# Optimization experiments

Measured on AMD Instinct MI355X. Metric: run time of the kernel, lower is better.

The kernel has to match this reference:

```python
import jax, jax.numpy as jnp
import numpy as np

CLASS_NUM = 31
KERNEL_MUL = 2.0
KERNEL_NUM = 5


def setup_inputs() -> dict:
    key = jax.random.key(0)
    k1, k2, k3, k4 = jax.random.split(key, 4)
    B, D = 4096, 512
    source = jax.random.normal(k1, (B, D), dtype=jnp.float32)
    target = jax.random.normal(k2, (B, D), dtype=jnp.float32)
    s_label = jax.random.randint(k3, (B,), 0, CLASS_NUM)
    t_label = jax.random.uniform(k4, (B, CLASS_NUM), dtype=jnp.float32)
    return {"source": source, "target": target, "s_label": s_label, "t_label": t_label}


def _cal_weight(s_label, t_label):
    # Faithful port of the numpy weight computation (detached in the original).
    C = CLASS_NUM
    s_onehot = jax.nn.one_hot(s_label, C, dtype=jnp.float32)          # [Bs, C]
    s_sum = s_onehot.sum(axis=0)
    s_vec = s_onehot / jnp.where(s_sum == 0, 1e9, s_sum)
    t_pred = jnp.argmax(t_label, axis=1)
    t_sum = t_label.sum(axis=0)
    t_vec = t_label / jnp.where(t_sum == 0, 1.0, t_sum)
    # classes present in BOTH source labels and target argmax predictions
    s_present = s_onehot.sum(axis=0) > 0
    t_present = jax.nn.one_hot(t_pred, C, dtype=jnp.float32).sum(axis=0) > 0
    mask = (s_present & t_present).astype(jnp.float32)                # [C]
    s_vec = s_vec * mask
    t_vec = t_vec * mask
    length = mask.sum()
    inv_len = jnp.where(length > 0, 1.0 / length, 0.0)
    w_ss = (s_vec @ s_vec.T) * inv_len
    w_tt = (t_vec @ t_vec.T) * inv_len
    w_st = (s_vec @ t_vec.T) * inv_len
    w_ts = (t_vec @ s_vec.T) * inv_len
    return w_ss, w_tt, w_st, w_ts


def _gaussian_kernel(source, target):
    n = source.shape[0] + target.shape[0]
    total = jnp.concatenate([source, target], axis=0)                 # [n, d]
    # Gram-matrix trick for pairwise squared L2 (avoids n x n x d intermediate)
    sq = jnp.sum(total * total, axis=1)                               # [n]
    L2 = jnp.maximum(sq[:, None] + sq[None, :] - 2.0 * (total @ total.T), 0.0)
    bandwidth = jax.lax.stop_gradient(jnp.sum(L2)) / (n * n - n)      # .data -> detach
    bandwidth = bandwidth / (KERNEL_MUL ** (KERNEL_NUM // 2))
    kernels = jnp.zeros_like(L2)
    for i in range(KERNEL_NUM):
        kernels = kernels + jnp.exp(-L2 / (bandwidth * KERNEL_MUL ** i))
    return kernels


def reference(source, target, s_label, t_label):
    B = source.shape[0]
    w_ss, w_tt, w_st, w_ts = _cal_weight(s_label, t_label)
    w_ss = jax.lax.stop_gradient(w_ss)
    w_tt = jax.lax.stop_gradient(w_tt)
    w_st = jax.lax.stop_gradient(w_st)
    w_ts = jax.lax.stop_gradient(w_ts)
    kernels = _gaussian_kernel(source, target)
    SS = kernels[:B, :B]
    TT = kernels[B:, B:]
    ST = kernels[:B, B:]
    TS = kernels[B:, :B]
    loss = (jnp.sum(w_ss * SS) + jnp.sum(w_tt * TT)
            - jnp.sum(w_st * ST) - jnp.sum(w_ts * TS))
    # original returns 0 if the kernel matrix contains NaNs
    return jnp.where(jnp.any(jnp.isnan(kernels)), 0.0, loss)
```

## Files before the change

kernel.cpp:

```cpp
#include <hip/hip_runtime.h>

#define N_TOT 8192
#define BHALF 4096
#define D 512
#define C 31
#define QS 21.166666666666668f
#define C2 0.0044644089288178575f

typedef float f32x16 __attribute__((ext_vector_type(16)));
typedef int   i32x16 __attribute__((ext_vector_type(16)));
typedef int   i32x4  __attribute__((ext_vector_type(4)));
typedef __bf16 bf16x8 __attribute__((ext_vector_type(8)));

__device__ __forceinline__ uint bf16_rne(uint u) {
  return (u + 0x7fffu + ((u >> 16) & 1u)) >> 16;
}
__device__ __forceinline__ void split2(float x, uint& h, uint& lo) {
  uint u = __float_as_uint(x);
  h = bf16_rne(u);
  float hf = __uint_as_float(h << 16);
  lo = bf16_rne(__float_as_uint(x - hf));
}
__device__ __forceinline__ void gll16(const void* g, void* s) {
  __builtin_amdgcn_global_load_lds(
      (const __attribute__((address_space(1))) unsigned int*)g,
      (__attribute__((address_space(3))) unsigned int*)s, 16, 0, 0);
}
__device__ __forceinline__ uint pack4(const float* x, int o) {
  uint r = 0;
  #pragma unroll
  for (int b = 0; b < 4; ++b) {
    float xs = x[o + b] * QS;
    xs = fmaxf(fminf(xs, 127.f), -127.f);
    int q = __float2int_rn(xs);
    r |= (uint)(q & 255) << (8 * b);
  }
  return r;
}

__global__ __launch_bounds__(256) void k_split(const float* __restrict__ src,
                                               const float* __restrict__ tgt,
                                               const float* __restrict__ tl,
                                               uchar* __restrict__ qG,
                                               float* __restrict__ sqp,
                                               float* __restrict__ tsum_p,
                                               int* __restrict__ pres_p) {
  __shared__ float lsq[4][32];
  __shared__ float ts[C];
  __shared__ int pr[32];
  int tid = threadIdx.x, l = tid & 63, wid = tid >> 6;
  int bx = (int)blockIdx.x;
  if (bx < 1024) {
    int rg = bx >> 2;
    int kb = bx & 3;
    int ksg = kb * 4 + wid;
    int row = rg * 32 + (l & 31);
    int k0 = ksg * 32 + (l >> 5) * 16;
    const float* p = (row < BHALF) ? src + (size_t)row * D : tgt + (size_t)(row - BHALF) * D;
    float x[16];
    #pragma unroll
    for (int q = 0; q < 4; ++q) {
      float4 v = *(const float4*)(p + k0 + q * 4);
      x[q*4+0] = v.x; x[q*4+1] = v.y; x[q*4+2] = v.z; x[q*4+3] = v.w;
    }
    uint4 o = make_uint4(pack4(x, 0), pack4(x, 4), pack4(x, 8), pack4(x, 12));
    *(uint4*)(qG + (((size_t)rg * 16 + ksg) * 64 + l) * 16) = o;
    float s = 0.f;
    #pragma unroll
    for (int j = 0; j < 16; ++j) s = fmaf(x[j], x[j], s);
    s += __shfl_xor(s, 32);
    if (l < 32) lsq[wid][l] = s;
    __syncthreads();
    if (tid < 32) {
      float t = lsq[0][tid] + lsq[1][tid] + lsq[2][tid] + lsq[3][tid];
      sqp[kb * 8192 + rg * 32 + tid] = t;
    }
  } else {
    int b = bx - 1024;
    if (tid < 32) { pr[tid] = 0; if (tid < C) ts[tid] = 0.f; }
    __syncthreads();
    int base = b * 128 * C;
    for (int idx = tid; idx < 128 * C; idx += 256) {
      atomicAdd(&ts[idx % C], tl[base + idx]);
    }
    if (tid < 128) {
      int row = b * 128 + tid;
      const float* p = tl + (size_t)row * C;
      float best = p[0]; int bi = 0;
      for (int c = 1; c < C; c++) { float v = p[c]; if (v > best) { best = v; bi = c; } }
      pr[bi] = 1;
    }
    __syncthreads();
    if (tid < 32) {
      tsum_p[b * 32 + tid] = (tid < C) ? ts[tid] : 0.f;
      pres_p[b * 32 + tid] = pr[tid];
    }
  }
}

__global__ __launch_bounds__(256) void k_prep(const float* __restrict__ sqp,
                                              const int* __restrict__ slab,
                                              const float* __restrict__ tsum_p,
                                              const int* __restrict__ pres_p,
                                              float* __restrict__ sq,
                                              float* __restrict__ sval,
                                              float* __restrict__ tscale,
                                              float* __restrict__ scal,
                                              float* __restrict__ out) {
  __shared__ float red[4];
  __shared__ int cnt[C];
  __shared__ float tsumS[32];
  __shared__ int presS[32];
  int tid = threadIdx.x;
  if (tid < C) cnt[tid] = 0;
  float s = 0.f;
  for (int it = 0; it < 32; ++it) {
    int row = it * 256 + tid;
    float v = sqp[row] + sqp[8192 + row] + sqp[16384 + row] + sqp[24576 + row];
    sq[row] = v;
    s += v;
  }
  #pragma unroll
  for (int off = 32; off; off >>= 1) s += __shfl_xor(s, off);
  if ((tid & 63) == 0) red[tid >> 6] = s;
  if (tid < 32) {
    float tv = 0.f; int prr = 0;
    for (int b = 0; b < 32; ++b) {
      tv += tsum_p[b * 32 + tid];
      prr |= pres_p[b * 32 + tid];
    }
    tsumS[tid] = tv; presS[tid] = prr;
  }
  for (int i = tid; i < BHALF; i += 256) atomicAdd(&cnt[slab[i]], 1);
  __syncthreads();
  if (tid == 0) {
    float S = red[0] + red[1] + red[2] + red[3];
    float sumL2 = 2.0f * (float)N_TOT * S;
    scal[0] = -1.4426950408889634f * 67100672.0f / (4.0f * sumL2);
    int len = 0;
    for (int c = 0; c < C; c++) {
      int mk = (cnt[c] > 0 && presS[c] != 0) ? 1 : 0;
      len += mk;
      sval[c] = mk ? (1.0f / (float)cnt[c]) : 0.0f;
      float tv = tsumS[c];
      tscale[c] = mk ? (1.0f / (tv == 0.0f ? 1.0f : tv)) : 0.0f;
    }
    scal[1] = (len > 0) ? (1.0f / (float)len) : 0.0f;
    out[0] = 0.f;
  }
}

__global__ __launch_bounds__(256, 3) void k_main(
    const uchar* __restrict__ qG,
    const int* __restrict__ slab, const float* __restrict__ tl,
    const float* __restrict__ sval, const float* __restrict__ tscale,
    const float* __restrict__ sq, const float* __restrict__ scal,
    float* __restrict__ out) {
  __shared__ uint4 As4[1024];
  __shared__ uint4 Bs4[1024];
  __shared__ float sqA[128], sqB[128], red[4];
  uchar* As = (uchar*)As4;
  uchar* Bs = (uchar*)Bs4;
  ushort* AsU = (ushort*)As4;
  ushort* BsU = (ushort*)Bs4;

  int tid = threadIdx.x;
  int l = tid & 63, wid = tid >> 6;

  int bid = (int)blockIdx.x;
  int swz = (bid & 7) * 260 + (bid >> 3);
  int ti = 0, rem = swz;
  for (;;) { int w = 64 - ti; if (rem < w) break; rem -= w; ++ti; }
  int tj = ti + rem;

  if (tid < 128) { sqA[tid] = sq[ti * 128 + tid]; sqB[tid] = sq[tj * 128 + tid]; }
  float nib = scal[0], invlen = scal[1];

  i32x16 zeroi;
  f32x16 zero16;
  #pragma unroll
  for (int k = 0; k < 16; ++k) { zeroi[k] = 0; zero16[k] = 0.f; }
  i32x16 acc[2][2];
  acc[0][0] = zeroi; acc[0][1] = zeroi; acc[1][0] = zeroi; acc[1][1] = zeroi;

  int wrg = (wid >> 1) * 2;
  int wcg = (wid & 1) * 2;

  int rgbase_m = ((wid < 2) ? ti : tj) * 4;
  int rg_off = (wid & 1) * 2;
  uchar* lb_m = (wid < 2) ? As : Bs;

  for (int kci = 0; kci < 8; ++kci) {
    #pragma unroll
    for (int r = 0; r < 4; ++r) {
      int rgl = rg_off + (r >> 1), ksl = r & 1;
      const uchar* g = qG + (((size_t)(rgbase_m + rgl) * 16 + kci * 2 + ksl) * 64 + l) * 16;
      gll16(g, lb_m + ((rgl * 2 + ksl) * 64 + l) * 16);
    }
    __syncthreads();
    __builtin_amdgcn_s_setprio(1);
    #pragma unroll
    for (int ksl = 0; ksl < 2; ++ksl) {
      i32x4 a0 = *(const i32x4*)(As + (((wrg + 0) * 2 + ksl) * 64 + l) * 16);
      i32x4 a1 = *(const i32x4*)(As + (((wrg + 1) * 2 + ksl) * 64 + l) * 16);
      i32x4 b0 = *(const i32x4*)(Bs + (((wcg + 0) * 2 + ksl) * 64 + l) * 16);
      i32x4 b1 = *(const i32x4*)(Bs + (((wcg + 1) * 2 + ksl) * 64 + l) * 16);
      acc[0][0] = __builtin_amdgcn_mfma_i32_32x32x32_i8(a0, b0, acc[0][0], 0, 0, 0);
      acc[0][1] = __builtin_amdgcn_mfma_i32_32x32x32_i8(a0, b1, acc[0][1], 0, 0, 0);
      acc[1][0] = __builtin_amdgcn_mfma_i32_32x32x32_i8(a1, b0, acc[1][0], 0, 0, 0);
      acc[1][1] = __builtin_amdgcn_mfma_i32_32x32x32_i8(a1, b1, acc[1][1], 0, 0, 0);
    }
    __builtin_amdgcn_s_setprio(0);
    __syncthreads();
  }

  #pragma unroll
  for (int it = 0; it < 4; ++it) {
    int slot = tid + it * 256;
    int pl = slot >> 6;
    int ll = slot & 63;
    int side = pl >> 3;
    int rgl = (pl & 7) >> 1;
    int ks = pl & 1;
    int row = (side ? tj : ti) * 128 + rgl * 32 + (ll & 31);
    int j0 = ks * 16 + (ll >> 5) * 8;
    float vals[8];
    if (row < BHALF) {
      int cls = slab[row];
      float v = sval[cls];
      #pragma unroll
      for (int jj = 0; jj < 8; ++jj) vals[jj] = (j0 + jj == cls) ? v : 0.f;
    } else {
      const float* p = tl + (size_t)(row - BHALF) * C;
      #pragma unroll
      for (int jj = 0; jj < 8; ++jj) {
        int cj = j0 + jj;
        vals[jj] = (cj < C) ? -p[cj] * tscale[cj] : 0.f;
      }
    }
    uint h[8], lo[8];
    #pragma unroll
    for (int jj = 0; jj < 8; ++jj) split2(vals[jj], h[jj], lo[jj]);
    ushort* base = (side ? BsU : AsU) + ((rgl * 2 + ks) * 64 + ll) * 8;
    *(uint4*)base = make_uint4(h[0]|(h[1]<<16), h[2]|(h[3]<<16),
                               h[4]|(h[5]<<16), h[6]|(h[7]<<16));
    *(uint4*)(base + 4096) = make_uint4(lo[0]|(lo[1]<<16), lo[2]|(lo[3]<<16),
                                        lo[4]|(lo[5]<<16), lo[6]|(lo[7]<<16));
  }
  __syncthreads();

  float partial = 0.f;
  int colb = (wid & 1) * 64 + (l & 31);
  int rowb = (wid >> 1) * 64 + 4 * (l >> 5);
  #pragma unroll
  for (int i = 0; i < 2; ++i) {
    bf16x8 caH0 = *(const bf16x8*)(AsU + (((wrg + i) * 2 + 0) * 64 + l) * 8);
    bf16x8 caH1 = *(const bf16x8*)(AsU + (((wrg + i) * 2 + 1) * 64 + l) * 8);
    bf16x8 caL0 = *(const bf16x8*)(AsU + 4096 + (((wrg + i) * 2 + 0) * 64 + l) * 8);
    bf16x8 caL1 = *(const bf16x8*)(AsU + 4096 + (((wrg + i) * 2 + 1) * 64 + l) * 8);
    #pragma unroll
    for (int j = 0; j < 2; ++j) {
      bf16x8 cbH0 = *(const bf16x8*)(BsU + (((wcg + j) * 2 + 0) * 64 + l) * 8);
      bf16x8 cbH1 = *(const bf16x8*)(BsU + (((wcg + j) * 2 + 1) * 64 + l) * 8);
      bf16x8 cbL0 = *(const bf16x8*)(BsU + 4096 + (((wcg + j) * 2 + 0) * 64 + l) * 8);
      bf16x8 cbL1 = *(const bf16x8*)(BsU + 4096 + (((wcg + j) * 2 + 1) * 64 + l) * 8);
      f32x16 w = zero16;
      w = __builtin_amdgcn_mfma_f32_32x32x16_bf16(caH0, cbH0, w, 0, 0, 0);
      w = __builtin_amdgcn_mfma_f32_32x32x16_bf16(caH1, cbH1, w, 0, 0, 0);
      w = __builtin_amdgcn_mfma_f32_32x32x16_bf16(caH0, cbL0, w, 0, 0, 0);
      w = __builtin_amdgcn_mfma_f32_32x32x16_bf16(caH1, cbL1, w, 0, 0, 0);
      w = __builtin_amdgcn_mfma_f32_32x32x16_bf16(caL0, cbH0, w, 0, 0, 0);
      w = __builtin_amdgcn_mfma_f32_32x32x16_bf16(caL1, cbH1, w, 0, 0, 0);
      float sb = sqB[colb + j * 32];
      #pragma unroll
      for (int reg = 0; reg < 16; ++reg) {
        int row = rowb + i * 32 + (reg & 3) + 8 * (reg >> 2);
        float l2 = fmaxf(sqA[row] + sb - C2 * (float)acc[i][j][reg], 0.f);
        float e = __builtin_amdgcn_exp2f(l2 * nib);
        float kern = e;
        e *= e; kern += e;
        e *= e; kern += e;
        e *= e; kern += e;
        e *= e; kern += e;
        partial = fmaf(w[reg], kern, partial);
      }
    }
  }
  #pragma unroll
  for (int off = 32; off; off >>= 1) partial += __shfl_xor(partial, off);
  if (l == 0) red[wid] = partial;
  __syncthreads();
  if (tid == 0) {
    float v = (red[0] + red[1] + red[2] + red[3]) * invlen * ((ti == tj) ? 1.0f : 2.0f);
    atomicAdd(out, v);
  }
}

extern "C" void kernel_launch(void* const* d_in, const int* in_sizes, int n_in,
                              void* d_out, int out_size, void* d_ws, size_t ws_size,
                              hipStream_t stream) {
  const float* src = (const float*)d_in[0];
  const float* tgt = (const float*)d_in[1];
  const int* slab  = (const int*)d_in[2];
  const float* tl  = (const float*)d_in[3];
  float* out = (float*)d_out;

  uchar*  qG = (uchar*)d_ws;
  float* fb  = (float*)(qG + 4194304);
  float* sqp    = fb;
  float* tsum_p = fb + 32768;
  int*   pres_p = (int*)(fb + 33792);
  float* sq     = fb + 34816;
  float* sval   = fb + 43008;
  float* tscale = fb + 43040;
  float* scal   = fb + 43072;

  hipLaunchKernelGGL(k_split, dim3(1056), dim3(256), 0, stream,
                     src, tgt, tl, qG, sqp, tsum_p, pres_p);
  hipLaunchKernelGGL(k_prep,  dim3(1),    dim3(256), 0, stream,
                     sqp, slab, tsum_p, pres_p, sq, sval, tscale, scal, out);
  hipLaunchKernelGGL(k_main,  dim3(2080), dim3(256), 0, stream,
                     qG, slab, tl, sval, tscale, sq, scal, out);
}
```

Before: 75.80 us.

## Merge split blocks per row group, fold bandwidth scale into sq, raise occupancy

k_split now has each block handle a full 32-row group across all K, looping four times, and writes final squared norms directly. This removes the partial-sum buffer and the reduction pass in k_prep. In k_main the bandwidth scale is folded into the sqA/sqB values and a single fma, which saves multiplies in the exp epilogue. The change also raises the launch-bounds occupancy hint from 3 to 4 and drops the s_setprio hints around the MFMA loop. The higher occupancy target may force register spills, and the k_split grid drops from 1056 to 288 blocks, which lowers its parallelism.

```diff
diff --git a/kernel.cpp b/kernel.cpp
--- a/kernel.cpp
+++ b/kernel.cpp
@@ -42,7 +42,7 @@
                                                const float* __restrict__ tgt,
                                                const float* __restrict__ tl,
                                                uchar* __restrict__ qG,
-                                               float* __restrict__ sqp,
+                                               float* __restrict__ sq,
                                                float* __restrict__ tsum_p,
                                                int* __restrict__ pres_p) {
   __shared__ float lsq[4][32];
@@ -50,33 +50,34 @@
   __shared__ int pr[32];
   int tid = threadIdx.x, l = tid & 63, wid = tid >> 6;
   int bx = (int)blockIdx.x;
-  if (bx < 1024) {
-    int rg = bx >> 2;
-    int kb = bx & 3;
-    int ksg = kb * 4 + wid;
+  if (bx < 256) {
+    int rg = bx;
     int row = rg * 32 + (l & 31);
-    int k0 = ksg * 32 + (l >> 5) * 16;
     const float* p = (row < BHALF) ? src + (size_t)row * D : tgt + (size_t)(row - BHALF) * D;
-    float x[16];
-    #pragma unroll
-    for (int q = 0; q < 4; ++q) {
-      float4 v = *(const float4*)(p + k0 + q * 4);
-      x[q*4+0] = v.x; x[q*4+1] = v.y; x[q*4+2] = v.z; x[q*4+3] = v.w;
-    }
-    uint4 o = make_uint4(pack4(x, 0), pack4(x, 4), pack4(x, 8), pack4(x, 12));
-    *(uint4*)(qG + (((size_t)rg * 16 + ksg) * 64 + l) * 16) = o;
     float s = 0.f;
     #pragma unroll
-    for (int j = 0; j < 16; ++j) s = fmaf(x[j], x[j], s);
+    for (int it = 0; it < 4; ++it) {
+      int ksg = wid + it * 4;
+      int k0 = ksg * 32 + (l >> 5) * 16;
+      float x[16];
+      #pragma unroll
+      for (int q = 0; q < 4; ++q) {
+        float4 v = *(const float4*)(p + k0 + q * 4);
+        x[q*4+0] = v.x; x[q*4+1] = v.y; x[q*4+2] = v.z; x[q*4+3] = v.w;
+      }
+      uint4 o = make_uint4(pack4(x, 0), pack4(x, 4), pack4(x, 8), pack4(x, 12));
+      *(uint4*)(qG + (((size_t)rg * 16 + ksg) * 64 + l) * 16) = o;
+      #pragma unroll
+      for (int j = 0; j < 16; ++j) s = fmaf(x[j], x[j], s);
+    }
     s += __shfl_xor(s, 32);
     if (l < 32) lsq[wid][l] = s;
     __syncthreads();
     if (tid < 32) {
-      float t = lsq[0][tid] + lsq[1][tid] + lsq[2][tid] + lsq[3][tid];
-      sqp[kb * 8192 + rg * 32 + tid] = t;
+      sq[rg * 32 + tid] = lsq[0][tid] + lsq[1][tid] + lsq[2][tid] + lsq[3][tid];
     }
   } else {
-    int b = bx - 1024;
+    int b = bx - 256;
     if (tid < 32) { pr[tid] = 0; if (tid < C) ts[tid] = 0.f; }
     __syncthreads();
     int base = b * 128 * C;
@@ -98,11 +99,10 @@
   }
 }
 
-__global__ __launch_bounds__(256) void k_prep(const float* __restrict__ sqp,
+__global__ __launch_bounds__(256) void k_prep(const float* __restrict__ sq,
                                               const int* __restrict__ slab,
                                               const float* __restrict__ tsum_p,
                                               const int* __restrict__ pres_p,
-                                              float* __restrict__ sq,
                                               float* __restrict__ sval,
                                               float* __restrict__ tscale,
                                               float* __restrict__ scal,
@@ -114,12 +114,7 @@
   int tid = threadIdx.x;
   if (tid < C) cnt[tid] = 0;
   float s = 0.f;
-  for (int it = 0; it < 32; ++it) {
-    int row = it * 256 + tid;
-    float v = sqp[row] + sqp[8192 + row] + sqp[16384 + row] + sqp[24576 + row];
-    sq[row] = v;
-    s += v;
-  }
+  for (int i = tid; i < N_TOT; i += 256) s += sq[i];
   #pragma unroll
   for (int off = 32; off; off >>= 1) s += __shfl_xor(s, off);
   if ((tid & 63) == 0) red[tid >> 6] = s;
@@ -150,7 +145,7 @@
   }
 }
 
-__global__ __launch_bounds__(256, 3) void k_main(
+__global__ __launch_bounds__(256, 4) void k_main(
     const uchar* __restrict__ qG,
     const int* __restrict__ slab, const float* __restrict__ tl,
     const float* __restrict__ sval, const float* __restrict__ tscale,
@@ -173,8 +168,9 @@
   for (;;) { int w = 64 - ti; if (rem < w) break; rem -= w; ++ti; }
   int tj = ti + rem;
 
-  if (tid < 128) { sqA[tid] = sq[ti * 128 + tid]; sqB[tid] = sq[tj * 128 + tid]; }
   float nib = scal[0], invlen = scal[1];
+  float c2n = -C2 * nib;
+  if (tid < 128) { sqA[tid] = sq[ti * 128 + tid] * nib; sqB[tid] = sq[tj * 128 + tid] * nib; }
 
   i32x16 zeroi;
   f32x16 zero16;
@@ -198,7 +194,6 @@
       gll16(g, lb_m + ((rgl * 2 + ksl) * 64 + l) * 16);
     }
     __syncthreads();
-    __builtin_amdgcn_s_setprio(1);
     #pragma unroll
     for (int ksl = 0; ksl < 2; ++ksl) {
       i32x4 a0 = *(const i32x4*)(As + (((wrg + 0) * 2 + ksl) * 64 + l) * 16);
@@ -210,7 +205,6 @@
       acc[1][0] = __builtin_amdgcn_mfma_i32_32x32x32_i8(a1, b0, acc[1][0], 0, 0, 0);
       acc[1][1] = __builtin_amdgcn_mfma_i32_32x32x32_i8(a1, b1, acc[1][1], 0, 0, 0);
     }
-    __builtin_amdgcn_s_setprio(0);
     __syncthreads();
   }
 
@@ -275,8 +269,9 @@
       #pragma unroll
       for (int reg = 0; reg < 16; ++reg) {
         int row = rowb + i * 32 + (reg & 3) + 8 * (reg >> 2);
-        float l2 = fmaxf(sqA[row] + sb - C2 * (float)acc[i][j][reg], 0.f);
-        float e = __builtin_amdgcn_exp2f(l2 * nib);
+        float g = fmaf(c2n, (float)acc[i][j][reg], sqA[row] + sb);
+        g = fminf(g, 0.f);
+        float e = __builtin_amdgcn_exp2f(g);
         float kern = e;
         e *= e; kern += e;
         e *= e; kern += e;
@@ -307,18 +302,17 @@
 
   uchar*  qG = (uchar*)d_ws;
   float* fb  = (float*)(qG + 4194304);
-  float* sqp    = fb;
-  float* tsum_p = fb + 32768;
-  int*   pres_p = (int*)(fb + 33792);
-  float* sq     = fb + 34816;
-  float* sval   = fb + 43008;
-  float* tscale = fb + 43040;
-  float* scal   = fb + 43072;
-
-  hipLaunchKernelGGL(k_split, dim3(1056), dim3(256), 0, stream,
-                     src, tgt, tl, qG, sqp, tsum_p, pres_p);
+  float* sq     = fb;
+  float* tsum_p = fb + 8192;
+  int*   pres_p = (int*)(fb + 9216);
+  float* sval   = fb + 10240;
+  float* tscale = fb + 10272;
+  float* scal   = fb + 10304;
+
+  hipLaunchKernelGGL(k_split, dim3(288),  dim3(256), 0, stream,
+                     src, tgt, tl, qG, sq, tsum_p, pres_p);
   hipLaunchKernelGGL(k_prep,  dim3(1),    dim3(256), 0, stream,
-                     sqp, slab, tsum_p, pres_p, sq, sval, tscale, scal, out);
+                     sq, slab, tsum_p, pres_p, sval, tscale, scal, out);
   hipLaunchKernelGGL(k_main,  dim3(2080), dim3(256), 0, stream,
                      qG, slab, tl, sval, tscale, sq, scal, out);
 }
```

Result: slower. 81.08 us (+7.0%).
